# Kernel optimization log

Measured on AMD Instinct MI355X. Metric: run time of the kernel, lower is better.

Reference implementation:

```python
import jax, jax.numpy as jnp
import numpy as np
from jax import lax

D_MODEL, D_STATE, D_CONV, EXPAND = 512, 16, 4, 2
D_INNER = EXPAND * D_MODEL          # 1024
DT_RANK = (D_MODEL + 15) // 16      # 32
BATCH, SEQ = 4, 1024


def setup_inputs() -> dict:
    key = jax.random.key(0)
    ks = jax.random.split(key, 8)
    s = 0.02
    x = jax.random.normal(ks[0], (BATCH, SEQ, D_MODEL), jnp.float32)
    in_proj_w = jax.random.normal(ks[1], (2 * D_INNER, D_MODEL), jnp.float32) * s
    conv_w = jax.random.normal(ks[2], (D_INNER, 1, D_CONV), jnp.float32) * s  # depthwise
    conv_b = jnp.zeros((D_INNER,), jnp.float32)
    x_proj_w = jax.random.normal(ks[3], (DT_RANK + 2 * D_STATE, D_INNER), jnp.float32) * s
    dt_proj_w = jax.random.normal(ks[4], (D_INNER, DT_RANK), jnp.float32) * s
    dt_proj_b = jax.random.normal(ks[5], (D_INNER,), jnp.float32) * 0.1
    # Mamba S4D-real init: A = -[1..d_state] per channel, stored as log
    A_log = jnp.log(jnp.tile(jnp.arange(1, D_STATE + 1, dtype=jnp.float32)[None, :], (D_INNER, 1)))
    D = jnp.ones((D_INNER,), jnp.float32)
    out_proj_w = jax.random.normal(ks[6], (D_MODEL, D_INNER), jnp.float32) * s
    ln_w = jnp.ones((D_MODEL,), jnp.float32)
    ln_b = jnp.zeros((D_MODEL,), jnp.float32)
    return dict(x=x, in_proj_w=in_proj_w, conv_w=conv_w, conv_b=conv_b,
                x_proj_w=x_proj_w, dt_proj_w=dt_proj_w, dt_proj_b=dt_proj_b,
                A_log=A_log, D=D, out_proj_w=out_proj_w, ln_w=ln_w, ln_b=ln_b)


def _selective_scan(u, delta, A, Bm, Cm, D):
    # u, delta: (B,L,Di); A: (Di,N); Bm, Cm: (B,L,N)
    dA = jnp.exp(delta[..., None] * A)                    # (B,L,Di,N)
    dBu = (delta * u)[..., None] * Bm[:, :, None, :]      # (B,L,Di,N)
    dA_t = jnp.moveaxis(dA, 1, 0)                         # (L,B,Di,N)
    dBu_t = jnp.moveaxis(dBu, 1, 0)
    C_t = jnp.moveaxis(Cm, 1, 0)                          # (L,B,N)

    def step(h, inp):
        dA_i, dBu_i, C_i = inp
        h = dA_i * h + dBu_i                              # (B,Di,N)
        y = jnp.einsum('bdn,bn->bd', h, C_i)
        return h, y

    h0 = jnp.zeros((u.shape[0], A.shape[0], A.shape[1]), u.dtype)
    _, ys = lax.scan(step, h0, (dA_t, dBu_t, C_t))        # ys: (L,B,Di)
    return jnp.moveaxis(ys, 0, 1) + u * D                 # (B,L,Di)


def reference(x, in_proj_w, conv_w, conv_b, x_proj_w, dt_proj_w, dt_proj_b,
              A_log, D, out_proj_w, ln_w, ln_b):
    # ---- Mamba SSM ----
    xz = jnp.einsum('bld,ed->ble', x, in_proj_w)          # (B,L,2*Di)
    xs, z = jnp.split(xz, 2, axis=-1)
    # causal depthwise conv over time
    xt = jnp.moveaxis(xs, 1, 2)                           # (B,Di,L)
    xt = lax.conv_general_dilated(xt, conv_w, window_strides=(1,),
                                  padding=[(D_CONV - 1, 0)],
                                  feature_group_count=D_INNER,
                                  dimension_numbers=('NCH', 'OIH', 'NCH'))
    xt = xt + conv_b[None, :, None]
    u = jax.nn.silu(jnp.moveaxis(xt, 1, 2))               # (B,L,Di)

    x_dbl = jnp.einsum('bld,ed->ble', u, x_proj_w)        # (B,L,dt_rank+2N)
    dt = x_dbl[..., :DT_RANK]
    Bm = x_dbl[..., DT_RANK:DT_RANK + D_STATE]
    Cm = x_dbl[..., DT_RANK + D_STATE:]
    delta = jax.nn.softplus(jnp.einsum('blr,dr->bld', dt, dt_proj_w) + dt_proj_b)
    A = -jnp.exp(A_log)                                   # (Di,N)

    y = _selective_scan(u, delta, A, Bm, Cm, D)
    y = y * jax.nn.silu(z)
    ssm_out = jnp.einsum('ble,de->bld', y, out_proj_w)    # (B,L,Dm)

    # ---- residual + LayerNorm ----
    r = x + ssm_out
    mu = jnp.mean(r, axis=-1, keepdims=True)
    var = jnp.mean(jnp.square(r - mu), axis=-1, keepdims=True)
    return (r - mu) / jnp.sqrt(var + 1e-5) * ln_w + ln_b
```

## Files before the change

kernel.cpp:

```cpp
#include <hip/hip_runtime.h>
#include <hip/hip_bf16.h>
#include <math.h>

#define B_   4
#define L_   1024
#define DM   512
#define DI   1024
#define NS   16
#define XDC  64
#define BL   4096
#define KS   4
#define CL   256
#define BCS  258

typedef short bfrag __attribute__((ext_vector_type(8)));
typedef float ffrag __attribute__((ext_vector_type(4)));

__device__ __forceinline__ ushort f2bf(float v) {
    __hip_bfloat16 h = __float2bfloat16(v);
    return *(ushort*)&h;
}

__global__ __launch_bounds__(256) void cast_bf16(const float* __restrict__ in,
        ushort* __restrict__ out, int n4)
{
    int i = blockIdx.x * 256 + threadIdx.x;
    if (i >= n4) return;
    float4 v = ((const float4*)in)[i];
    ushort4 o;
    o.x = f2bf(v.x); o.y = f2bf(v.y); o.z = f2bf(v.z); o.w = f2bf(v.w);
    ((ushort4*)out)[i] = o;
}

template<int EPI>
__global__ __launch_bounds__(256) void gemm_mfma(const ushort* __restrict__ A,
        const ushort* __restrict__ B, float* __restrict__ C,
        int K, int ldc, const float* __restrict__ resid,
        const float* __restrict__ bias)
{
    __shared__ ushort As[128][40];
    __shared__ ushort Bs[128][40];
    const int tid = threadIdx.x;
    const int lane = tid & 63, wave = tid >> 6;
    const int wm = (wave & 1) * 64, wn = (wave >> 1) * 64;
    const int l15 = lane & 15, quad = lane >> 4;
    const int m0 = blockIdx.y * 128, n0 = blockIdx.x * 128;

    ffrag acc[4][4] = {};

    for (int k0 = 0; k0 < K; k0 += 32) {
        #pragma unroll
        for (int i = 0; i < 2; i++) {
            int chunk = tid + i * 256;
            int row = chunk >> 2, kk8 = (chunk & 3) * 8;
            *(uint4*)&As[row][kk8] = *(const uint4*)&A[(size_t)(m0 + row) * K + k0 + kk8];
            *(uint4*)&Bs[row][kk8] = *(const uint4*)&B[(size_t)(n0 + row) * K + k0 + kk8];
        }
        __syncthreads();
        bfrag af[4], bfv[4];
        #pragma unroll
        for (int i = 0; i < 4; i++) {
            af[i]  = *(const bfrag*)&As[wm + i * 16 + l15][quad * 8];
            bfv[i] = *(const bfrag*)&Bs[wn + i * 16 + l15][quad * 8];
        }
        #pragma unroll
        for (int i = 0; i < 4; i++)
            #pragma unroll
            for (int j = 0; j < 4; j++)
                acc[i][j] = __builtin_amdgcn_mfma_f32_16x16x32_bf16(af[i], bfv[j], acc[i][j], 0, 0, 0);
        __syncthreads();
    }

    #pragma unroll
    for (int i = 0; i < 4; i++) {
        #pragma unroll
        for (int j = 0; j < 4; j++) {
            int n = n0 + wn + j * 16 + l15;
            #pragma unroll
            for (int r = 0; r < 4; r++) {
                int m = m0 + wm + i * 16 + quad * 4 + r;
                float v = acc[i][j][r];
                if (EPI == 2) v += resid[(size_t)m * ldc + n];
                C[(size_t)m * ldc + n] = v;
            }
        }
    }
}

__global__ __launch_bounds__(256) void gemm3_splitk(const float* __restrict__ uT,
        const float* __restrict__ xw, float* __restrict__ part)
{
    __shared__ float As[16][33];
    __shared__ float Ws[16][68];
    const int tid = threadIdx.x;
    const int tx = tid & 15, ty = tid >> 4;
    const int ks = blockIdx.x, m0 = blockIdx.y * 32;
    const int kbase = ks * (DI / KS);
    float acc[2][4] = {};

    for (int k0 = 0; k0 < DI / KS; k0 += 16) {
        if (tid < 128) {
            int k = tid >> 3, m4 = (tid & 7) * 4;
            const float4 v = *(const float4*)&uT[(size_t)(kbase + k0 + k) * BL + m0 + m4];
            As[k][m4 + 0] = v.x; As[k][m4 + 1] = v.y;
            As[k][m4 + 2] = v.z; As[k][m4 + 3] = v.w;
        }
        {
            int r = tid >> 2, c4 = (tid & 3) * 4;
            const float4 v = *(const float4*)&xw[(size_t)r * DI + kbase + k0 + c4];
            Ws[c4 + 0][r] = v.x; Ws[c4 + 1][r] = v.y;
            Ws[c4 + 2][r] = v.z; Ws[c4 + 3][r] = v.w;
        }
        __syncthreads();
        #pragma unroll
        for (int kk = 0; kk < 16; kk++) {
            float a[2], b[4];
            a[0] = As[kk][ty * 2 + 0];
            a[1] = As[kk][ty * 2 + 1];
            #pragma unroll
            for (int j = 0; j < 4; j++) b[j] = Ws[kk][tx * 4 + j];
            #pragma unroll
            for (int i = 0; i < 2; i++)
                #pragma unroll
                for (int j = 0; j < 4; j++)
                    acc[i][j] = fmaf(a[i], b[j], acc[i][j]);
        }
        __syncthreads();
    }

    float* pp = part + (size_t)ks * BL * XDC;
    #pragma unroll
    for (int i = 0; i < 2; i++) {
        int m = m0 + ty * 2 + i;
        *(float4*)&pp[(size_t)m * XDC + tx * 4] =
            make_float4(acc[i][0], acc[i][1], acc[i][2], acc[i][3]);
    }
}

__global__ __launch_bounds__(256) void gemm3_reduce(const float* __restrict__ part,
        float* __restrict__ xdbl)
{
    int i = blockIdx.x * 256 + threadIdx.x;
    const float4* p0 = (const float4*)part;
    float4 a = p0[i];
    #pragma unroll
    for (int s = 1; s < KS; s++) {
        float4 b = p0[i + (size_t)s * BL * XDC / 4];
        a.x += b.x; a.y += b.y; a.z += b.z; a.w += b.w;
    }
    ((float4*)xdbl)[i] = a;
}

__global__ __launch_bounds__(256) void dt_softplus(const float* __restrict__ xdbl,
        const float* __restrict__ dtw, const float* __restrict__ bias,
        float* __restrict__ deltaT)
{
    __shared__ float dts[256][33];
    const int tid = threadIdx.x;
    const int lane = tid & 63;
    const int bl0 = blockIdx.x * 256;

    {
        const float4* src = (const float4*)(xdbl + (size_t)(bl0 + tid) * XDC);
        #pragma unroll
        for (int k = 0; k < 8; k++) {
            float4 v = src[k];
            *(float4*)&dts[tid][k * 4] = v;
        }
    }

    int d = blockIdx.y * 4 + (tid >> 6);
    d = __builtin_amdgcn_readfirstlane(d);
    float wreg[32];
    {
        const float4* wp = (const float4*)(dtw + (size_t)d * 32);
        #pragma unroll
        for (int k = 0; k < 8; k++) *(float4*)&wreg[k * 4] = wp[k];
    }
    const float bb = bias[d];
    __syncthreads();

    #pragma unroll
    for (int s = 0; s < 4; s++) {
        const int bl = s * 64 + lane;
        float acc = bb;
        #pragma unroll
        for (int k = 0; k < 8; k++) {
            float4 v = *(const float4*)&dts[bl][k * 4];
            acc = fmaf(wreg[k * 4 + 0], v.x, acc);
            acc = fmaf(wreg[k * 4 + 1], v.y, acc);
            acc = fmaf(wreg[k * 4 + 2], v.z, acc);
            acc = fmaf(wreg[k * 4 + 3], v.w, acc);
        }
        float outv = (acc > 20.f) ? acc : __logf(1.f + __expf(acc));
        deltaT[(size_t)d * BL + bl0 + bl] = outv;
    }
}

__global__ __launch_bounds__(256) void conv_silu(const float* __restrict__ xzT,
        const float* __restrict__ cw, const float* __restrict__ cb,
        float* __restrict__ uT)
{
    int i = blockIdx.x * 256 + threadIdx.x;
    int d  = i >> 10;
    int q  = i & 1023;
    int bl = q * 4;
    int l  = bl & (L_ - 1);
    const float* row = xzT + (size_t)d * BL;
    float4 cur = *(const float4*)&row[bl];
    float4 prev = make_float4(0.f, 0.f, 0.f, 0.f);
    if (l != 0) prev = *(const float4*)&row[bl - 4];
    float v[7] = { prev.y, prev.z, prev.w, cur.x, cur.y, cur.z, cur.w };
    float w0 = cw[d * 4 + 0], w1 = cw[d * 4 + 1], w2 = cw[d * 4 + 2], w3 = cw[d * 4 + 3];
    float bias = cb[d];
    float4 o;
    o.x = bias + w0 * v[0] + w1 * v[1] + w2 * v[2] + w3 * v[3];
    o.y = bias + w0 * v[1] + w1 * v[2] + w2 * v[3] + w3 * v[4];
    o.z = bias + w0 * v[2] + w1 * v[3] + w2 * v[4] + w3 * v[5];
    o.w = bias + w0 * v[3] + w1 * v[4] + w2 * v[5] + w3 * v[6];
    o.x = o.x / (1.f + __expf(-o.x));
    o.y = o.y / (1.f + __expf(-o.y));
    o.z = o.z / (1.f + __expf(-o.z));
    o.w = o.w / (1.f + __expf(-o.w));
    *(float4*)&uT[(size_t)d * BL + bl] = o;
}

__global__ __launch_bounds__(256) void scan_fused(const float* __restrict__ deltaT,
        const float* __restrict__ uT, const float* __restrict__ xdbl,
        const float* __restrict__ xzT, const float* __restrict__ A_log,
        const float* __restrict__ Dp, float* __restrict__ yT)
{
    __shared__ float bc[32 * BCS];

    const int tid = threadIdx.x;
    const int lane = tid & 63;
    const int bd = blockIdx.x * 4 + (tid >> 6);
    const int d = bd & (DI - 1);
    const int b = bd >> 10;

    float Acoef[16];
    {
        const float4* ap = (const float4*)(A_log + d * NS);
        #pragma unroll
        for (int i = 0; i < 4; i++) {
            float4 v = ap[i];
            Acoef[i * 4 + 0] = -__expf(v.x); Acoef[i * 4 + 1] = -__expf(v.y);
            Acoef[i * 4 + 2] = -__expf(v.z); Acoef[i * 4 + 3] = -__expf(v.w);
        }
    }
    const float Dd = Dp[d];

    const size_t row_t = (size_t)d * BL + b * L_;
    const size_t row_z = (size_t)(DI + d) * BL + b * L_;

    float h[16];
    #pragma unroll
    for (int n = 0; n < 16; n++) h[n] = 0.f;

    for (int c = 0; c < L_ / CL; c++) {
        __syncthreads();
        {
            const float* src = xdbl + ((size_t)b * L_ + c * CL) * XDC + 32;
            #pragma unroll
            for (int i = 0; i < 8; i++) {
                int idx = tid + i * 256;
                int l = idx >> 3, c4 = idx & 7;
                float4 v = *(const float4*)&src[(size_t)l * XDC + c4 * 4];
                int n0 = c4 * 4;
                bc[(n0 + 0) * BCS + l] = v.x;
                bc[(n0 + 1) * BCS + l] = v.y;
                bc[(n0 + 2) * BCS + l] = v.z;
                bc[(n0 + 3) * BCS + l] = v.w;
            }
        }
        __syncthreads();

        const int l0 = c * CL + lane * 4;
        const int lb = lane * 4;
        float4 dvv = *(const float4*)&deltaT[row_t + l0];
        float4 uvv = *(const float4*)&uT[row_t + l0];
        float dv[4] = { dvv.x, dvv.y, dvv.z, dvv.w };
        float du[4] = { dvv.x * uvv.x, dvv.y * uvv.y, dvv.z * uvv.z, dvv.w * uvv.w };
        float sa = dv[0] + dv[1] + dv[2] + dv[3];

        float a[16], bb[16];
        #pragma unroll
        for (int n = 0; n < 16; n++) {
            a[n] = __expf(sa * Acoef[n]);
            const float4 Bv = *(const float4*)&bc[n * BCS + lb];
            float acc = du[0] * Bv.x;
            acc = fmaf(__expf(dv[1] * Acoef[n]), acc, du[1] * Bv.y);
            acc = fmaf(__expf(dv[2] * Acoef[n]), acc, du[2] * Bv.z);
            acc = fmaf(__expf(dv[3] * Acoef[n]), acc, du[3] * Bv.w);
            bb[n] = acc;
        }

        #pragma unroll
        for (int off = 1; off < 64; off <<= 1) {
            #pragma unroll
            for (int n = 0; n < 16; n++) {
                float pa = __shfl_up(a[n], off);
                float pb = __shfl_up(bb[n], off);
                if (lane >= off) {
                    bb[n] = fmaf(a[n], pb, bb[n]);
                    a[n] *= pa;
                }
            }
        }

        #pragma unroll
        for (int n = 0; n < 16; n++) {
            float pa = __shfl_up(a[n], 1);
            float pb = __shfl_up(bb[n], 1);
            float ae = (lane == 0) ? 1.f : pa;
            float be = (lane == 0) ? 0.f : pb;
            h[n] = fmaf(ae, h[n], be);
        }

        float s0 = 0.f, s1 = 0.f, s2 = 0.f, s3 = 0.f;
        #pragma unroll
        for (int n = 0; n < 16; n++) {
            const float4 Bv = *(const float4*)&bc[n * BCS + lb];
            const float4 Cv = *(const float4*)&bc[(16 + n) * BCS + lb];
            float hn = h[n];
            hn = fmaf(__expf(dv[0] * Acoef[n]), hn, du[0] * Bv.x);
            s0 = fmaf(hn, Cv.x, s0);
            hn = fmaf(__expf(dv[1] * Acoef[n]), hn, du[1] * Bv.y);
            s1 = fmaf(hn, Cv.y, s1);
            hn = fmaf(__expf(dv[2] * Acoef[n]), hn, du[2] * Bv.z);
            s2 = fmaf(hn, Cv.z, s2);
            hn = fmaf(__expf(dv[3] * Acoef[n]), hn, du[3] * Bv.w);
            s3 = fmaf(hn, Cv.w, s3);
            h[n] = hn;
        }

        #pragma unroll
        for (int n = 0; n < 16; n++) h[n] = __shfl(h[n], 63);

        float4 zv = *(const float4*)&xzT[row_z + l0];
        float4 yv;
        float v0 = s0 + uvv.x * Dd; yv.x = v0 * (zv.x / (1.f + __expf(-zv.x)));
        float v1 = s1 + uvv.y * Dd; yv.y = v1 * (zv.y / (1.f + __expf(-zv.y)));
        float v2 = s2 + uvv.z * Dd; yv.z = v2 * (zv.z / (1.f + __expf(-zv.z)));
        float v3 = s3 + uvv.w * Dd; yv.w = v3 * (zv.w / (1.f + __expf(-zv.w)));
        *(float4*)&yT[row_t + l0] = yv;
    }
}

__global__ __launch_bounds__(256) void transpose_cast(const float* __restrict__ yT,
        ushort* __restrict__ yB)
{
    __shared__ float t[64][65];
    const int bl0 = blockIdx.x * 64, d0 = blockIdx.y * 64;
    const int tid = threadIdx.x;
    #pragma unroll
    for (int i = 0; i < 4; i++) {
        int chunk = tid + i * 256;
        int dr = chunk >> 4, c4 = (chunk & 15) * 4;
        const float4 v = *(const float4*)&yT[(size_t)(d0 + dr) * BL + bl0 + c4];
        t[dr][c4 + 0] = v.x; t[dr][c4 + 1] = v.y;
        t[dr][c4 + 2] = v.z; t[dr][c4 + 3] = v.w;
    }
    __syncthreads();
    #pragma unroll
    for (int i = 0; i < 4; i++) {
        int chunk = tid + i * 256;
        int br = chunk >> 4, dc4 = (chunk & 15) * 4;
        ushort4 o;
        o.x = f2bf(t[dc4 + 0][br]); o.y = f2bf(t[dc4 + 1][br]);
        o.z = f2bf(t[dc4 + 2][br]); o.w = f2bf(t[dc4 + 3][br]);
        *(ushort4*)&yB[(size_t)(bl0 + br) * DI + d0 + dc4] = o;
    }
}

__global__ __launch_bounds__(256) void ln_kernel(const float* __restrict__ r,
        const float* __restrict__ lnw, const float* __restrict__ lnb,
        float* __restrict__ out)
{
    int row = blockIdx.x;
    const float* rr = r + (size_t)row * DM;
    float v0 = rr[threadIdx.x], v1 = rr[threadIdx.x + 256];
    float s = v0 + v1, s2 = v0 * v0 + v1 * v1;
    #pragma unroll
    for (int off = 32; off > 0; off >>= 1) {
        s  += __shfl_down(s, off);
        s2 += __shfl_down(s2, off);
    }
    __shared__ float ls[4], ls2[4];
    __shared__ float mu_s, rstd_s;
    int wid = threadIdx.x >> 6, lane = threadIdx.x & 63;
    if (lane == 0) { ls[wid] = s; ls2[wid] = s2; }
    __syncthreads();
    if (threadIdx.x == 0) {
        float S = ls[0] + ls[1] + ls[2] + ls[3];
        float S2 = ls2[0] + ls2[1] + ls2[2] + ls2[3];
        float mu = S * (1.f / DM);
        float var = S2 * (1.f / DM) - mu * mu;
        mu_s = mu;
        rstd_s = rsqrtf(var + 1e-5f);
    }
    __syncthreads();
    float mu = mu_s, rstd = rstd_s;
    out[(size_t)row * DM + threadIdx.x] =
        (v0 - mu) * rstd * lnw[threadIdx.x] + lnb[threadIdx.x];
    out[(size_t)row * DM + threadIdx.x + 256] =
        (v1 - mu) * rstd * lnw[threadIdx.x + 256] + lnb[threadIdx.x + 256];
}

extern "C" void kernel_launch(void* const* d_in, const int* in_sizes, int n_in,
                              void* d_out, int out_size, void* d_ws, size_t ws_size,
                              hipStream_t stream)
{
    const float* x         = (const float*)d_in[0];
    const float* in_proj_w = (const float*)d_in[1];
    const float* conv_w    = (const float*)d_in[2];
    const float* conv_b    = (const float*)d_in[3];
    const float* x_proj_w  = (const float*)d_in[4];
    const float* dt_proj_w = (const float*)d_in[5];
    const float* dt_proj_b = (const float*)d_in[6];
    const float* A_log     = (const float*)d_in[7];
    const float* Dvec      = (const float*)d_in[8];
    const float* out_proj_w= (const float*)d_in[9];
    const float* ln_w      = (const float*)d_in[10];
    const float* ln_b      = (const float*)d_in[11];
    float* out = (float*)d_out;

    float* ws     = (float*)d_ws;
    float* xzT    = ws;
    float* uT     = xzT    + (size_t)2048 * BL;
    float* xdbl   = uT     + (size_t)DI * BL;
    float* deltaT = xdbl   + (size_t)BL * XDC;
    float* yT     = deltaT + (size_t)DI * BL;
    float* r      = yT     + (size_t)DI * BL;
    ushort* xB    = (ushort*)yT;
    float*  xdblp = yT;
    ushort* yB    = (ushort*)deltaT;
    ushort* wOutB = (ushort*)deltaT + (size_t)4 * 1024 * 1024;
    ushort* wInB  = (ushort*)deltaT + (size_t)9 * 1024 * 1024 / 2;

    dim3 blk(256);

    cast_bf16<<<(BL * DM / 4 + 255) / 256, blk, 0, stream>>>(x, xB, BL * DM / 4);
    cast_bf16<<<(2048 * DM / 4 + 255) / 256, blk, 0, stream>>>(in_proj_w, wInB, 2048 * DM / 4);

    gemm_mfma<0><<<dim3(BL / 128, 2048 / 128), blk, 0, stream>>>(
        wInB, xB, xzT, DM, BL, nullptr, nullptr);

    conv_silu<<<(DI * BL / 4) / 256, blk, 0, stream>>>(xzT, conv_w, conv_b, uT);

    gemm3_splitk<<<dim3(KS, BL / 32), blk, 0, stream>>>(uT, x_proj_w, xdblp);
    gemm3_reduce<<<(BL * XDC / 4) / 256, blk, 0, stream>>>(xdblp, xdbl);

    dt_softplus<<<dim3(BL / 256, DI / 4), blk, 0, stream>>>(
        xdbl, dt_proj_w, dt_proj_b, deltaT);

    scan_fused<<<B_ * DI / 4, blk, 0, stream>>>(
        deltaT, uT, xdbl, xzT, A_log, Dvec, yT);

    transpose_cast<<<dim3(BL / 64, DI / 64), blk, 0, stream>>>(yT, yB);
    cast_bf16<<<(DM * DI / 4 + 255) / 256, blk, 0, stream>>>(out_proj_w, wOutB, DM * DI / 4);

    gemm_mfma<2><<<dim3(DM / 128, BL / 128), blk, 0, stream>>>(
        yB, wOutB, r, DI, DM, x, nullptr);

    ln_kernel<<<BL, blk, 0, stream>>>(r, ln_w, ln_b, out);
}
```

Baseline: 267.8 us.

## Fuse fp32-to-bf16 casts into GEMM tile loads; widen scan blocks to 512 threads

Drops the three separate cast_bf16 launches by having the MFMA GEMM read fp32 inputs directly and convert to bf16 while staging tiles into shared memory. This removes the extra kernel launches and the round trip of writing and re-reading bf16 copies through global memory. The cost is that each GEMM tile load now reads twice the bytes and converts them, repeatedly across output tiles. The scan kernel also moves to 512-thread blocks (8 channels per block), so each B/C chunk staged in shared memory is shared by more channels.

```diff
diff --git a/kernel.cpp b/kernel.cpp
--- a/kernel.cpp
+++ b/kernel.cpp
@@ -21,22 +21,23 @@
     return *(ushort*)&h;
 }
 
-__global__ __launch_bounds__(256) void cast_bf16(const float* __restrict__ in,
-        ushort* __restrict__ out, int n4)
-{
-    int i = blockIdx.x * 256 + threadIdx.x;
-    if (i >= n4) return;
-    float4 v = ((const float4*)in)[i];
-    ushort4 o;
-    o.x = f2bf(v.x); o.y = f2bf(v.y); o.z = f2bf(v.z); o.w = f2bf(v.w);
-    ((ushort4*)out)[i] = o;
-}
-
-template<int EPI>
-__global__ __launch_bounds__(256) void gemm_mfma(const ushort* __restrict__ A,
-        const ushort* __restrict__ B, float* __restrict__ C,
-        int K, int ldc, const float* __restrict__ resid,
-        const float* __restrict__ bias)
+template<bool F32>
+__device__ __forceinline__ void stage8(const void* p, size_t eoff, ushort* dst) {
+    if constexpr (F32) {
+        const float* f = (const float*)p + eoff;
+        float4 v0 = *(const float4*)f;
+        float4 v1 = *(const float4*)(f + 4);
+        *(ushort4*)dst       = make_ushort4(f2bf(v0.x), f2bf(v0.y), f2bf(v0.z), f2bf(v0.w));
+        *(ushort4*)(dst + 4) = make_ushort4(f2bf(v1.x), f2bf(v1.y), f2bf(v1.z), f2bf(v1.w));
+    } else {
+        *(uint4*)dst = *(const uint4*)((const ushort*)p + eoff);
+    }
+}
+
+template<int EPI, bool AF, bool BF>
+__global__ __launch_bounds__(256) void gemm_mfma(const void* __restrict__ Ap,
+        const void* __restrict__ Bp, float* __restrict__ C,
+        int K, int ldc, const float* __restrict__ resid)
 {
     __shared__ ushort As[128][40];
     __shared__ ushort Bs[128][40];
@@ -53,8 +54,8 @@
         for (int i = 0; i < 2; i++) {
             int chunk = tid + i * 256;
             int row = chunk >> 2, kk8 = (chunk & 3) * 8;
-            *(uint4*)&As[row][kk8] = *(const uint4*)&A[(size_t)(m0 + row) * K + k0 + kk8];
-            *(uint4*)&Bs[row][kk8] = *(const uint4*)&B[(size_t)(n0 + row) * K + k0 + kk8];
+            stage8<AF>(Ap, (size_t)(m0 + row) * K + k0 + kk8, &As[row][kk8]);
+            stage8<BF>(Bp, (size_t)(n0 + row) * K + k0 + kk8, &Bs[row][kk8]);
         }
         __syncthreads();
         bfrag af[4], bfv[4];
@@ -225,7 +226,7 @@
     *(float4*)&uT[(size_t)d * BL + bl] = o;
 }
 
-__global__ __launch_bounds__(256) void scan_fused(const float* __restrict__ deltaT,
+__global__ __launch_bounds__(512) void scan_fused(const float* __restrict__ deltaT,
         const float* __restrict__ uT, const float* __restrict__ xdbl,
         const float* __restrict__ xzT, const float* __restrict__ A_log,
         const float* __restrict__ Dp, float* __restrict__ yT)
@@ -234,7 +235,7 @@
 
     const int tid = threadIdx.x;
     const int lane = tid & 63;
-    const int bd = blockIdx.x * 4 + (tid >> 6);
+    const int bd = blockIdx.x * 8 + (tid >> 6);
     const int d = bd & (DI - 1);
     const int b = bd >> 10;
 
@@ -262,8 +263,8 @@
         {
             const float* src = xdbl + ((size_t)b * L_ + c * CL) * XDC + 32;
             #pragma unroll
-            for (int i = 0; i < 8; i++) {
-                int idx = tid + i * 256;
+            for (int i = 0; i < 4; i++) {
+                int idx = tid + i * 512;
                 int l = idx >> 3, c4 = idx & 7;
                 float4 v = *(const float4*)&src[(size_t)l * XDC + c4 * 4];
                 int n0 = c4 * 4;
@@ -432,19 +433,13 @@
     float* deltaT = xdbl   + (size_t)BL * XDC;
     float* yT     = deltaT + (size_t)DI * BL;
     float* r      = yT     + (size_t)DI * BL;
-    ushort* xB    = (ushort*)yT;
     float*  xdblp = yT;
     ushort* yB    = (ushort*)deltaT;
-    ushort* wOutB = (ushort*)deltaT + (size_t)4 * 1024 * 1024;
-    ushort* wInB  = (ushort*)deltaT + (size_t)9 * 1024 * 1024 / 2;
 
     dim3 blk(256);
 
-    cast_bf16<<<(BL * DM / 4 + 255) / 256, blk, 0, stream>>>(x, xB, BL * DM / 4);
-    cast_bf16<<<(2048 * DM / 4 + 255) / 256, blk, 0, stream>>>(in_proj_w, wInB, 2048 * DM / 4);
-
-    gemm_mfma<0><<<dim3(BL / 128, 2048 / 128), blk, 0, stream>>>(
-        wInB, xB, xzT, DM, BL, nullptr, nullptr);
+    gemm_mfma<0, true, true><<<dim3(BL / 128, 2048 / 128), blk, 0, stream>>>(
+        in_proj_w, x, xzT, DM, BL, nullptr);
 
     conv_silu<<<(DI * BL / 4) / 256, blk, 0, stream>>>(xzT, conv_w, conv_b, uT);
 
@@ -454,14 +449,13 @@
     dt_softplus<<<dim3(BL / 256, DI / 4), blk, 0, stream>>>(
         xdbl, dt_proj_w, dt_proj_b, deltaT);
 
-    scan_fused<<<B_ * DI / 4, blk, 0, stream>>>(
+    scan_fused<<<B_ * DI / 8, dim3(512), 0, stream>>>(
         deltaT, uT, xdbl, xzT, A_log, Dvec, yT);
 
     transpose_cast<<<dim3(BL / 64, DI / 64), blk, 0, stream>>>(yT, yB);
-    cast_bf16<<<(DM * DI / 4 + 255) / 256, blk, 0, stream>>>(out_proj_w, wOutB, DM * DI / 4);
-
-    gemm_mfma<2><<<dim3(DM / 128, BL / 128), blk, 0, stream>>>(
-        yB, wOutB, r, DI, DM, x, nullptr);
+
+    gemm_mfma<2, false, true><<<dim3(DM / 128, BL / 128), blk, 0, stream>>>(
+        yB, out_proj_w, r, DI, DM, x);
 
     ln_kernel<<<BL, blk, 0, stream>>>(r, ln_w, ln_b, out);
 }
```

Result: slower. 275.1 us (+2.7%).
